# Kernel tuning notes

Hardware: AMD Instinct MI355X
Metric: run time of the kernel (lower is better)

Reference implementation:

```python
import jax, jax.numpy as jnp
import numpy as np

CHUNK_FRAMES = 100
LOOKAHEAD_FRAMES = 50
NUM_HEADS = 16


def _allowed_mask(T):
    # frame i attends to j iff chunk(j) <= chunk(i) OR j <= i + lookahead
    pos = jnp.arange(T)
    chunk = pos // CHUNK_FRAMES
    chunk_ok = chunk[None, :] <= chunk[:, None]          # (T, T) keys per query row
    look_ok = pos[None, :] <= pos[:, None] + LOOKAHEAD_FRAMES
    return chunk_ok | look_ok                             # bool (T, T)


def setup_inputs() -> dict:
    key = jax.random.key(0)
    ks = jax.random.split(key, 8)
    B, T, D = 4, 1500, 1024
    s = 1.0 / np.sqrt(D)
    return {
        "hidden_states": jax.random.normal(ks[0], (B, T, D), jnp.float32),
        "Wq": jax.random.normal(ks[1], (D, D), jnp.float32) * s,
        "bq": jax.random.normal(ks[2], (D,), jnp.float32) * 0.02,
        "Wk": jax.random.normal(ks[3], (D, D), jnp.float32) * s,
        "Wv": jax.random.normal(ks[4], (D, D), jnp.float32) * s,
        "bv": jax.random.normal(ks[5], (D,), jnp.float32) * 0.02,
        "Wo": jax.random.normal(ks[6], (D, D), jnp.float32) * s,
        "bo": jax.random.normal(ks[7], (D,), jnp.float32) * 0.02,
    }


def reference(hidden_states, Wq, bq, Wk, Wv, bv, Wo, bo):
    B, T, D = hidden_states.shape
    H = NUM_HEADS
    hd = D // H
    scale = hd ** -0.5

    # Whisper attention: q scaled, k_proj has no bias
    q = (hidden_states @ Wq + bq) * scale       # (B, T, D)
    k = hidden_states @ Wk                       # (B, T, D)
    v = hidden_states @ Wv + bv                  # (B, T, D)

    q = q.reshape(B, T, H, hd)
    k = k.reshape(B, T, H, hd)
    v = v.reshape(B, T, H, hd)

    scores = jnp.einsum("bqhd,bkhd->bhqk", q, k)  # (B, H, T, T)
    allowed = _allowed_mask(T)                     # (T, T)
    neg = jnp.asarray(jnp.finfo(scores.dtype).min, scores.dtype)
    scores = jnp.where(allowed[None, None, :, :], scores, neg)

    attn = jax.nn.softmax(scores, axis=-1)
    out = jnp.einsum("bhqk,bkhd->bqhd", attn, v).reshape(B, T, D)
    return out @ Wo + bo
```

## Files before the change

kernel.cpp:

```cpp
#include <hip/hip_runtime.h>


typedef unsigned short u16;
typedef unsigned int   u32;
typedef unsigned long long u64;
typedef __attribute__((ext_vector_type(8))) short bf16x8;
typedef __attribute__((ext_vector_type(4))) float f32x4;

typedef const __attribute__((address_space(1))) u32 gu32;
typedef __attribute__((address_space(3))) u32 lu32;

__device__ __forceinline__ void load_lds16(void* lds, const void* g) {
    __builtin_amdgcn_global_load_lds((gu32*)g, (lu32*)lds, 16, 0, 0);
}

__device__ __forceinline__ u16 f2bf(float x) {
    u32 u = __builtin_bit_cast(u32, x);
    u = (u + 0x7fffu + ((u >> 16) & 1u)) >> 16;
    return (u16)u;
}

#define NTOK 6000

__global__ __launch_bounds__(256) void wa_cvt_x(const float* __restrict__ X,
                                                u16* __restrict__ Xb) {
    size_t i = ((size_t)blockIdx.x * 256 + threadIdx.x) * 4;
    if (i >= (size_t)6144000) return;
    float4 v = *(const float4*)(X + i);
    u64 p = (u64)f2bf(v.x) | ((u64)f2bf(v.y) << 16)
          | ((u64)f2bf(v.z) << 32) | ((u64)f2bf(v.w) << 48);
    *(u64*)(Xb + i) = p;
}

__global__ __launch_bounds__(256) void wa_pack_w(const float* __restrict__ Wq,
                                                 const float* __restrict__ Wk,
                                                 const float* __restrict__ Wv,
                                                 const float* __restrict__ Wo,
                                                 u16* __restrict__ Wt,
                                                 u16* __restrict__ Wto) {
    __shared__ float tile[64][65];
    const int n0 = blockIdx.x * 64;
    const int k0 = blockIdx.y * 64;
    const float* src; u16* dst; int cn;
    if (n0 < 3072) {
        int sel = n0 >> 10;
        src = (sel == 0) ? Wq : ((sel == 1) ? Wk : Wv);
        cn = n0 & 1023;
        dst = Wt + (size_t)n0 * 1024;
    } else {
        src = Wo; cn = n0 - 3072;
        dst = Wto + (size_t)(n0 - 3072) * 1024;
    }
    const int t = threadIdx.x;
    #pragma unroll
    for (int i = 0; i < 16; i++) {
        int idx = t + i * 256;
        int r = idx >> 6, c = idx & 63;
        tile[r][c] = src[(size_t)(k0 + r) * 1024 + cn + c];
    }
    __syncthreads();
    #pragma unroll
    for (int i = 0; i < 16; i++) {
        int idx = t + i * 256;
        int nr = idx >> 6, kc = idx & 63;
        dst[(size_t)nr * 1024 + k0 + kc] = f2bf(tile[kc][nr]);
    }
}

template<int EPI>
__global__ __launch_bounds__(256) void wa_gemm(
        const u16* __restrict__ A, const u16* __restrict__ Bt,
        const float* __restrict__ bq, const float* __restrict__ bv,
        u16* __restrict__ Qb, u16* __restrict__ Kb, u16* __restrict__ Vt,
        const float* __restrict__ bo, float* __restrict__ outF) {
    __shared__ u16 As[128 * 32];
    __shared__ u16 Bs[128 * 32];
    const int tid = threadIdx.x;
    const int wave = tid >> 6, lane = tid & 63;
    const int wm = wave >> 1, wn = wave & 1;
    const int r = lane & 15, g = lane >> 4;
    const int m0 = blockIdx.x * 128, n0 = blockIdx.y * 128;
    const bool swp = (EPI == 1) || (n0 < 2048);

    const f32x4 z4 = {0.f, 0.f, 0.f, 0.f};
    f32x4 acc[4][4];
    #pragma unroll
    for (int i = 0; i < 4; i++)
        #pragma unroll
        for (int j = 0; j < 4; j++)
            acc[i][j] = z4;

    const int srow = wave * 32 + (lane >> 2);
    const int scol = (lane & 3) * 8;
    const u16* aSrc = A + (size_t)(m0 + srow) * 1024 + scol;
    const u16* bSrc = Bt + (size_t)(n0 + srow) * 1024 + scol;
    char* aDst = (char*)As + wave * 2048;
    char* bDst = (char*)Bs + wave * 2048;

    for (int k0 = 0; k0 < 1024; k0 += 32) {
        __syncthreads();
        load_lds16(aDst,        aSrc + k0);
        load_lds16(aDst + 1024, aSrc + 16 * 1024 + k0);
        load_lds16(bDst,        bSrc + k0);
        load_lds16(bDst + 1024, bSrc + 16 * 1024 + k0);
        __syncthreads();
        bf16x8 a[4], b[4];
        #pragma unroll
        for (int i = 0; i < 4; i++)
            a[i] = *(const bf16x8*)&As[(wm * 64 + i * 16 + r) * 32 + g * 8];
        #pragma unroll
        for (int j = 0; j < 4; j++)
            b[j] = *(const bf16x8*)&Bs[(wn * 64 + j * 16 + r) * 32 + g * 8];
        if (swp) {
            #pragma unroll
            for (int i = 0; i < 4; i++)
                #pragma unroll
                for (int j = 0; j < 4; j++)
                    acc[i][j] = __builtin_amdgcn_mfma_f32_16x16x32_bf16(b[j], a[i], acc[i][j], 0, 0, 0);
        } else {
            #pragma unroll
            for (int i = 0; i < 4; i++)
                #pragma unroll
                for (int j = 0; j < 4; j++)
                    acc[i][j] = __builtin_amdgcn_mfma_f32_16x16x32_bf16(a[i], b[j], acc[i][j], 0, 0, 0);
        }
    }

    if constexpr (EPI == 0) {
        const int sel = n0 >> 10;
        if (sel < 2) {
            #pragma unroll
            for (int i = 0; i < 4; i++) {
                int gm = m0 + wm * 64 + i * 16 + r;
                if (gm >= NTOK) continue;
                int bb = gm / 1500, tt = gm - bb * 1500;
                #pragma unroll
                for (int j = 0; j < 4; j++) {
                    int w0 = (n0 & 1023) + wn * 64 + j * 16 + g * 4;
                    int h = w0 >> 6, d0 = w0 & 63;
                    u16* dst = (sel == 0 ? Qb : Kb)
                             + ((size_t)(bb * 16 + h) * 1500 + tt) * 64 + d0;
                    u64 pk;
                    if (sel == 0) {
                        float4 bqv = *(const float4*)(bq + w0);
                        pk = (u64)f2bf((acc[i][j][0] + bqv.x) * 0.125f)
                           | ((u64)f2bf((acc[i][j][1] + bqv.y) * 0.125f) << 16)
                           | ((u64)f2bf((acc[i][j][2] + bqv.z) * 0.125f) << 32)
                           | ((u64)f2bf((acc[i][j][3] + bqv.w) * 0.125f) << 48);
                    } else {
                        pk = (u64)f2bf(acc[i][j][0])
                           | ((u64)f2bf(acc[i][j][1]) << 16)
                           | ((u64)f2bf(acc[i][j][2]) << 32)
                           | ((u64)f2bf(acc[i][j][3]) << 48);
                    }
                    *(u64*)dst = pk;
                }
            }
        } else {
            #pragma unroll
            for (int j = 0; j < 4; j++) {
                int gn = n0 + wn * 64 + j * 16 + r;
                int w = gn & 1023;
                int h = w >> 6, d = w & 63;
                float bias = bv[w];
                #pragma unroll
                for (int i = 0; i < 4; i++) {
                    int gm0 = m0 + wm * 64 + i * 16 + g * 4;
                    if (gm0 >= NTOK) continue;
                    int bb = gm0 / 1500, tt0 = gm0 - bb * 1500;
                    u64 pk = (u64)f2bf(acc[i][j][0] + bias)
                           | ((u64)f2bf(acc[i][j][1] + bias) << 16)
                           | ((u64)f2bf(acc[i][j][2] + bias) << 32)
                           | ((u64)f2bf(acc[i][j][3] + bias) << 48);
                    *(u64*)(Vt + ((size_t)(bb * 16 + h) * 64 + d) * 1504 + tt0) = pk;
                }
            }
        }
    } else {
        #pragma unroll
        for (int i = 0; i < 4; i++) {
            int gm = m0 + wm * 64 + i * 16 + r;
            if (gm >= NTOK) continue;
            #pragma unroll
            for (int j = 0; j < 4; j++) {
                int gn0 = n0 + wn * 64 + j * 16 + g * 4;
                float4 bov = *(const float4*)(bo + gn0);
                float4 v = {acc[i][j][0] + bov.x, acc[i][j][1] + bov.y,
                            acc[i][j][2] + bov.z, acc[i][j][3] + bov.w};
                *(float4*)(outF + (size_t)gm * 1024 + gn0) = v;
            }
        }
    }
}

__global__ __launch_bounds__(256) void wa_attn(const u16* __restrict__ Qb,
                                               const u16* __restrict__ Kb,
                                               const u16* __restrict__ Vt,
                                               u16* __restrict__ Ob) {
    __shared__ u16 Ks[64 * 64];
    __shared__ u16 Vs[64 * 64];
    __shared__ u16 Ps[4][16 * 64];
    const int tid = threadIdx.x, wave = tid >> 6, lane = tid & 63;
    const int q = lane & 15, g = lane >> 4;
    const int qt = blockIdx.x, h = blockIdx.y, b = blockIdx.z;
    const int plane = b * 16 + h;

    const int qr = qt * 64 + wave * 16 + q;
    const int qc = qr < 1500 ? qr : 1499;
    int Lq = (qr / 100 + 1) * 100;
    { int la = qr + 51; if (la > Lq) Lq = la; }
    if (Lq > 1500) Lq = 1500;
    int qmax = qt * 64 + 63; if (qmax > 1499) qmax = 1499;
    int Lb = (qmax / 100 + 1) * 100;
    { int lb2 = qmax + 51; if (lb2 > Lb) Lb = lb2; }
    if (Lb > 1500) Lb = 1500;

    const u16* qp = Qb + ((size_t)plane * 1500 + qc) * 64 + g * 8;
    const bf16x8 qa0 = *(const bf16x8*)qp;
    const bf16x8 qa1 = *(const bf16x8*)(qp + 32);

    const f32x4 z4 = {0.f, 0.f, 0.f, 0.f};
    f32x4 accO[4];
    #pragma unroll
    for (int dt = 0; dt < 4; dt++) accO[dt] = z4;
    float m_run = -3.0e38f, l_run = 0.f;

    const int kRow0 = wave * 16 + (lane >> 3);
    const int kO = (lane & 7) * 16;

    for (int j0 = 0; j0 < Lb; j0 += 64) {
        __syncthreads();
        #pragma unroll
        for (int i = 0; i < 2; i++) {
            int row = kRow0 + i * 8;
            int so = kO ^ ((row & 7) << 4);
            int key = j0 + row; if (key > 1499) key = 1499;
            load_lds16((char*)Ks + wave * 2048 + i * 1024,
                       Kb + ((size_t)plane * 1500 + key) * 64 + (so >> 1));
            int vc = j0 + (so >> 1);
            if (vc > 1496) vc = 1496;
            load_lds16((char*)Vs + wave * 2048 + i * 1024,
                       Vt + ((size_t)plane * 64 + row) * 1504 + vc);
        }
        __syncthreads();

        f32x4 st[4];
        #pragma unroll
        for (int t = 0; t < 4; t++) {
            f32x4 s = z4;
            #pragma unroll
            for (int ks = 0; ks < 2; ks++) {
                int krow = t * 16 + q;
                int cb = (ks * 64 + g * 16) ^ ((krow & 7) << 4);
                bf16x8 kf = *(const bf16x8*)((const char*)Ks + krow * 128 + cb);
                s = __builtin_amdgcn_mfma_f32_16x16x32_bf16(kf, ks ? qa1 : qa0, s, 0, 0, 0);
            }
            st[t] = s;
        }

        float p[16];
        float mt = -3.0e38f;
        #pragma unroll
        for (int t = 0; t < 4; t++)
            #pragma unroll
            for (int e = 0; e < 4; e++) {
                int key = j0 + t * 16 + g * 4 + e;
                float sv = (key < Lq) ? st[t][e] : -3.0e38f;
                p[t * 4 + e] = sv;
                mt = fmaxf(mt, sv);
            }
        mt = fmaxf(mt, __shfl_xor(mt, 16));
        mt = fmaxf(mt, __shfl_xor(mt, 32));
        float m_new = fmaxf(m_run, mt);
        float resc = __expf(m_run - m_new);
        float sum = 0.f;
        #pragma unroll
        for (int i = 0; i < 16; i++) { p[i] = __expf(p[i] - m_new); sum += p[i]; }
        sum += __shfl_xor(sum, 16);
        sum += __shfl_xor(sum, 32);
        l_run = l_run * resc + sum;
        m_run = m_new;
        #pragma unroll
        for (int dt = 0; dt < 4; dt++) accO[dt] *= resc;

        {
            char* pw = (char*)Ps[wave];
            const int sw = (q & 7) << 4;
            #pragma unroll
            for (int t = 0; t < 4; t++) {
                u32 lo = (u32)f2bf(p[t * 4 + 0]) | ((u32)f2bf(p[t * 4 + 1]) << 16);
                u32 hi = (u32)f2bf(p[t * 4 + 2]) | ((u32)f2bf(p[t * 4 + 3]) << 16);
                int c0 = t * 32 + g * 8;
                *(u32*)(pw + q * 128 + ((c0)     ^ sw)) = lo;
                *(u32*)(pw + q * 128 + ((c0 + 4) ^ sw)) = hi;
            }
        }
        asm volatile("" ::: "memory");

        #pragma unroll
        for (int s2 = 0; s2 < 2; s2++) {
            int cb = s2 * 64 + g * 16;
            bf16x8 pf = *(const bf16x8*)((const char*)Ps[wave] + q * 128 + (cb ^ ((q & 7) << 4)));
            #pragma unroll
            for (int dt = 0; dt < 4; dt++) {
                int dr = dt * 16 + q;
                bf16x8 vf = *(const bf16x8*)((const char*)Vs + dr * 128 + (cb ^ ((dr & 7) << 4)));
                accO[dt] = __builtin_amdgcn_mfma_f32_16x16x32_bf16(vf, pf, accO[dt], 0, 0, 0);
            }
        }
    }

    float inv = 1.0f / l_run;
    if (qr < 1500) {
        u16* op = Ob + ((size_t)(b * 1500 + qr)) * 1024 + h * 64;
        #pragma unroll
        for (int dt = 0; dt < 4; dt++)
            #pragma unroll
            for (int e = 0; e < 4; e++)
                op[dt * 16 + g * 4 + e] = f2bf(accO[dt][e] * inv);
    }
}

extern "C" void kernel_launch(void* const* d_in, const int* in_sizes, int n_in,
                              void* d_out, int out_size, void* d_ws, size_t ws_size,
                              hipStream_t stream) {
    (void)in_sizes; (void)n_in; (void)out_size; (void)ws_size;
    const float* X  = (const float*)d_in[0];
    const float* Wq = (const float*)d_in[1];
    const float* bq = (const float*)d_in[2];
    const float* Wk = (const float*)d_in[3];
    const float* Wv = (const float*)d_in[4];
    const float* bv = (const float*)d_in[5];
    const float* Wo = (const float*)d_in[6];
    const float* bo = (const float*)d_in[7];
    float* out = (float*)d_out;

    u16* Xb  = (u16*)d_ws;
    u16* Wt  = Xb  + (size_t)6016 * 1024;
    u16* Wto = Wt  + (size_t)3072 * 1024;
    u16* Qb  = Wto + (size_t)1024 * 1024;
    u16* Kb  = Qb  + (size_t)64 * 1500 * 64;
    u16* Vt  = Kb  + (size_t)64 * 1500 * 64;

    wa_cvt_x<<<6000, 256, 0, stream>>>(X, Xb);
    wa_pack_w<<<dim3(64, 16), 256, 0, stream>>>(Wq, Wk, Wv, Wo, Wt, Wto);
    wa_gemm<0><<<dim3(47, 24), 256, 0, stream>>>(Xb, Wt, bq, bv, Qb, Kb, Vt, nullptr, nullptr);
    wa_attn<<<dim3(24, 16, 4), 256, 0, stream>>>(Qb, Kb, Vt, Xb);
    wa_gemm<1><<<dim3(47, 8), 256, 0, stream>>>(Xb, Wto, nullptr, nullptr, nullptr, nullptr, nullptr, bo, out);
}
```

Baseline: 198.1 us.

## Double-buffer K/V tiles in attention, remap blocks across planes, vectorize output stores

The attention kernel now keeps two LDS buffers for K and V and issues the next tile's async global-to-LDS loads before computing on the current tile, so each iteration needs one barrier instead of two and load latency can overlap the MFMA work. The grid becomes 1D with a block-index remap that interleaves 8 planes per query tile, which changes the dispatch order and likely how K/V data is shared in cache. Output stores are packed into 64-bit writes. The cost is twice the LDS for K/V, which may lower occupancy.

```diff
diff --git a/kernel.cpp b/kernel.cpp
--- a/kernel.cpp
+++ b/kernel.cpp
@@ -197,13 +197,15 @@
                                                const u16* __restrict__ Kb,
                                                const u16* __restrict__ Vt,
                                                u16* __restrict__ Ob) {
-    __shared__ u16 Ks[64 * 64];
-    __shared__ u16 Vs[64 * 64];
+    __shared__ u16 Ks[2][64 * 64];
+    __shared__ u16 Vs[2][64 * 64];
     __shared__ u16 Ps[4][16 * 64];
     const int tid = threadIdx.x, wave = tid >> 6, lane = tid & 63;
     const int q = lane & 15, g = lane >> 4;
-    const int qt = blockIdx.x, h = blockIdx.y, b = blockIdx.z;
-    const int plane = b * 16 + h;
+    const int bid = blockIdx.x;
+    const int qt = (bid >> 3) % 24;
+    const int plane = ((bid >> 3) / 24) * 8 + (bid & 7);
+    const int h = plane & 15, b = plane >> 4;
 
     const int qr = qt * 64 + wave * 16 + q;
     const int qc = qr < 1500 ? qr : 1499;
@@ -214,6 +216,7 @@
     int Lb = (qmax / 100 + 1) * 100;
     { int lb2 = qmax + 51; if (lb2 > Lb) Lb = lb2; }
     if (Lb > 1500) Lb = 1500;
+    const int ntiles = (Lb + 63) >> 6;
 
     const u16* qp = Qb + ((size_t)plane * 1500 + qc) * 64 + g * 8;
     const bf16x8 qa0 = *(const bf16x8*)qp;
@@ -225,24 +228,34 @@
     for (int dt = 0; dt < 4; dt++) accO[dt] = z4;
     float m_run = -3.0e38f, l_run = 0.f;
 
-    const int kRow0 = wave * 16 + (lane >> 3);
-    const int kO = (lane & 7) * 16;
-
-    for (int j0 = 0; j0 < Lb; j0 += 64) {
-        __syncthreads();
-        #pragma unroll
-        for (int i = 0; i < 2; i++) {
-            int row = kRow0 + i * 8;
-            int so = kO ^ ((row & 7) << 4);
-            int key = j0 + row; if (key > 1499) key = 1499;
-            load_lds16((char*)Ks + wave * 2048 + i * 1024,
-                       Kb + ((size_t)plane * 1500 + key) * 64 + (so >> 1));
-            int vc = j0 + (so >> 1);
-            if (vc > 1496) vc = 1496;
-            load_lds16((char*)Vs + wave * 2048 + i * 1024,
-                       Vt + ((size_t)plane * 64 + row) * 1504 + vc);
-        }
-        __syncthreads();
+    const int sRow = wave * 16 + (lane >> 3);
+    const int sO = (lane & 7) * 16;
+    const u16* kBase = Kb + (size_t)plane * 1500 * 64;
+    const u16* vBase = Vt + (size_t)plane * 64 * 1504;
+
+#define STAGE(J0, BUF) do {                                              \
+        _Pragma("unroll")                                                \
+        for (int i_ = 0; i_ < 2; i_++) {                                 \
+            int row_ = sRow + i_ * 8;                                    \
+            int so_ = sO ^ ((row_ & 7) << 4);                            \
+            int key_ = (J0) + row_; if (key_ > 1499) key_ = 1499;        \
+            load_lds16((char*)Ks[BUF] + wave * 2048 + i_ * 1024,         \
+                       kBase + (size_t)key_ * 64 + (so_ >> 1));          \
+            int vc_ = (J0) + (so_ >> 1); if (vc_ > 1496) vc_ = 1496;     \
+            load_lds16((char*)Vs[BUF] + wave * 2048 + i_ * 1024,         \
+                       vBase + (size_t)row_ * 1504 + vc_);               \
+        } } while (0)
+
+    STAGE(0, 0);
+    __syncthreads();
+    int cur = 0;
+
+    for (int ti = 0; ti < ntiles; ti++) {
+        const int j0 = ti << 6;
+        if (ti + 1 < ntiles) STAGE(j0 + 64, cur ^ 1);
+
+        const char* kb = (const char*)Ks[cur];
+        const char* vb = (const char*)Vs[cur];
 
         f32x4 st[4];
         #pragma unroll
@@ -252,7 +265,7 @@
             for (int ks = 0; ks < 2; ks++) {
                 int krow = t * 16 + q;
                 int cb = (ks * 64 + g * 16) ^ ((krow & 7) << 4);
-                bf16x8 kf = *(const bf16x8*)((const char*)Ks + krow * 128 + cb);
+                bf16x8 kf = *(const bf16x8*)(kb + krow * 128 + cb);
                 s = __builtin_amdgcn_mfma_f32_16x16x32_bf16(kf, ks ? qa1 : qa0, s, 0, 0, 0);
             }
             st[t] = s;
@@ -304,20 +317,27 @@
             #pragma unroll
             for (int dt = 0; dt < 4; dt++) {
                 int dr = dt * 16 + q;
-                bf16x8 vf = *(const bf16x8*)((const char*)Vs + dr * 128 + (cb ^ ((dr & 7) << 4)));
+                bf16x8 vf = *(const bf16x8*)(vb + dr * 128 + (cb ^ ((dr & 7) << 4)));
                 accO[dt] = __builtin_amdgcn_mfma_f32_16x16x32_bf16(vf, pf, accO[dt], 0, 0, 0);
             }
         }
-    }
+
+        __syncthreads();
+        cur ^= 1;
+    }
+#undef STAGE
 
     float inv = 1.0f / l_run;
     if (qr < 1500) {
-        u16* op = Ob + ((size_t)(b * 1500 + qr)) * 1024 + h * 64;
-        #pragma unroll
-        for (int dt = 0; dt < 4; dt++)
-            #pragma unroll
-            for (int e = 0; e < 4; e++)
-                op[dt * 16 + g * 4 + e] = f2bf(accO[dt][e] * inv);
+        u16* op = Ob + ((size_t)(b * 1500 + qr)) * 1024 + h * 64 + g * 4;
+        #pragma unroll
+        for (int dt = 0; dt < 4; dt++) {
+            u64 pk = (u64)f2bf(accO[dt][0] * inv)
+                   | ((u64)f2bf(accO[dt][1] * inv) << 16)
+                   | ((u64)f2bf(accO[dt][2] * inv) << 32)
+                   | ((u64)f2bf(accO[dt][3] * inv) << 48);
+            *(u64*)(op + dt * 16) = pk;
+        }
     }
 }
 
@@ -345,6 +365,6 @@
     wa_cvt_x<<<6000, 256, 0, stream>>>(X, Xb);
     wa_pack_w<<<dim3(64, 16), 256, 0, stream>>>(Wq, Wk, Wv, Wo, Wt, Wto);
     wa_gemm<0><<<dim3(47, 24), 256, 0, stream>>>(Xb, Wt, bq, bv, Qb, Kb, Vt, nullptr, nullptr);
-    wa_attn<<<dim3(24, 16, 4), 256, 0, stream>>>(Qb, Kb, Vt, Xb);
+    wa_attn<<<1536, 256, 0, stream>>>(Qb, Kb, Vt, Xb);
     wa_gemm<1><<<dim3(47, 8), 256, 0, stream>>>(Xb, Wto, nullptr, nullptr, nullptr, nullptr, nullptr, bo, out);
 }
```

After: 193.1 us. 1.03x faster.
